# Performance work log

Measured on AMD Instinct MI355X. Metric: run time of the kernel, lower is better.

Reference implementation:

```python
import jax, jax.numpy as jnp
import numpy as np

B, T, DIN, E, H, P = 8, 2048, 256, 256, 4, 8
HD = E // H


def _xavier(key, out_dim, in_dim):
    lim = float(np.sqrt(6.0 / (in_dim + out_dim)))
    return jax.random.uniform(key, (out_dim, in_dim), jnp.float32, -lim, lim)


def setup_inputs() -> dict:
    key = jax.random.key(0)
    ks = jax.random.split(key, 9)
    return {
        "x": jax.random.normal(ks[0], (B, T, DIN), jnp.float32),
        "w_in": _xavier(ks[1], E, DIN), "b_in": jnp.zeros((E,), jnp.float32),
        # MHA in-projections (torch packs qkv; xavier over packed [3E,E] approximated per-slice)
        "w_q": _xavier(ks[2], E, E), "b_q": jnp.zeros((E,), jnp.float32),
        "w_k": _xavier(ks[3], E, E), "b_k": jnp.zeros((E,), jnp.float32),
        "w_v": _xavier(ks[4], E, E), "b_v": jnp.zeros((E,), jnp.float32),
        "w_o": _xavier(ks[5], E, E), "b_o": jnp.zeros((E,), jnp.float32),
        "w_bd": _xavier(ks[6], 1, E), "b_bd": jnp.zeros((1,), jnp.float32),
        "w_pr": _xavier(ks[7], E, E), "b_pr": jnp.zeros((E,), jnp.float32),
    }


def reference(x, w_in, b_in, w_q, b_q, w_k, b_k, w_v, b_v, w_o, b_o, w_bd, b_bd, w_pr, b_pr):
    b, t, _ = x.shape
    h = x @ w_in.T + b_in                                   # [B,T,E]
    # self-attention (batch_first MHA, eval mode -> dropout is identity)
    q = (h @ w_q.T + b_q).reshape(b, t, H, HD)
    k = (h @ w_k.T + b_k).reshape(b, t, H, HD)
    v = (h @ w_v.T + b_v).reshape(b, t, H, HD)
    scale = 1.0 / np.sqrt(HD).astype(np.float32)
    scores = jnp.einsum("bqhd,bkhd->bhqk", q * scale, k)   # [B,H,T,T]
    attn = jax.nn.softmax(scores, axis=-1)
    ao = jnp.einsum("bhqk,bkhd->bqhd", attn, v).reshape(b, t, E)
    ao = ao @ w_o.T + b_o
    # boundary scoring -> dynamic patch ids
    bs = jax.nn.sigmoid(ao @ w_bd.T + b_bd)[..., 0]         # [B,T]
    cum = jnp.cumsum(bs, axis=1)
    normalized = cum / jnp.maximum(cum[:, -1:], 1e-6)
    pid = jnp.minimum((normalized * P).astype(jnp.int32), P - 1)  # [B,T]
    # mean-pool h into P dynamic patches (scatter_add + counts, via one-hot segment matmul)
    oh = jax.nn.one_hot(pid, P, dtype=h.dtype)              # [B,T,P]
    patch_emb = jnp.einsum("btp,btd->bpd", oh, h)           # [B,P,E]
    counts = oh.sum(axis=1)[..., None]                      # [B,P,1]
    patch_emb = patch_emb / jnp.maximum(counts, 1.0)
    return patch_emb @ w_pr.T + b_pr                        # [B,P,E]
```

## Files before the change

### kernel.cpp

```cpp
#include <hip/hip_runtime.h>
#include <cstddef>

#define NB 8
#define NT 2048
#define NE 256
#define NH 4
#define ND 64
#define NP 8

typedef short bf16x8 __attribute__((ext_vector_type(8)));
typedef float f32x4 __attribute__((ext_vector_type(4)));

__device__ __forceinline__ unsigned short f2bf(float f) {
  unsigned u = __builtin_bit_cast(unsigned, f);
  u += 0x7fffu + ((u >> 16) & 1u);
  return (unsigned short)(u >> 16);
}
__device__ __forceinline__ float bf2f(unsigned short h) {
  unsigned u = ((unsigned)h) << 16;
  return __builtin_bit_cast(float, u);
}
__device__ __forceinline__ void split2(float a, float b, unsigned& hi, unsigned& lo) {
  const unsigned short ha = f2bf(a), hb = f2bf(b);
  hi = (unsigned)ha | ((unsigned)hb << 16);
  const unsigned short la = f2bf(a - bf2f(ha));
  const unsigned short lb = f2bf(b - bf2f(hb));
  lo = (unsigned)la | ((unsigned)lb << 16);
}
__device__ __forceinline__ void gld16(const void* g, void* l) {
  __builtin_amdgcn_global_load_lds((const __attribute__((address_space(1))) unsigned*)g,
                                   (__attribute__((address_space(3))) unsigned*)l, 16, 0, 0);
}

#define QSC 0.180336880111120419f

__global__ __launch_bounds__(256) void setup1_kernel(
    const float* __restrict__ w_o, const float* __restrict__ b_o,
    const float* __restrict__ w_bd, const float* __restrict__ b_bd,
    const float* __restrict__ w_v, const float* __restrict__ b_v,
    float* __restrict__ uvbuf, float* __restrict__ consts)
{
  __shared__ float wbd_s[NE];
  __shared__ float u_s[NE];
  const int tid = threadIdx.x;
  wbd_s[tid] = w_bd[tid];
  __syncthreads();
  float a = 0.f;
  for (int j = 0; j < NE; ++j) a = fmaf(wbd_s[j], w_o[j * NE + tid], a);
  u_s[tid] = a;
  __syncthreads();
  #pragma unroll
  for (int hh = 0; hh < NH; ++hh) {
    float a2 = 0.f;
    for (int d = 0; d < ND; ++d)
      a2 = fmaf(u_s[hh * ND + d], w_v[(size_t)(hh * ND + d) * NE + tid], a2);
    uvbuf[hh * NE + tid] = a2;
  }
  if (tid == 0) {
    float cc = 0.f;
    for (int j = 0; j < NE; ++j) cc = fmaf(wbd_s[j], b_o[j], cc);
    consts[0] = cc + b_bd[0];
  }
  if (tid >= 8 && tid < 12) {
    const int hh = tid - 8;
    float cv = 0.f;
    for (int d = 0; d < ND; ++d) cv = fmaf(u_s[hh * ND + d], b_v[hh * ND + d], cv);
    consts[1 + hh] = cv;
  }
}

__global__ __launch_bounds__(256) void setup2_kernel(
    const float* __restrict__ w_in, const float* __restrict__ w_q,
    const float* __restrict__ w_k, const float* __restrict__ b_in,
    const float* __restrict__ b_q, const float* __restrict__ b_k,
    const float* __restrict__ uvbuf, const float* __restrict__ consts,
    unsigned short* __restrict__ wfhi, unsigned short* __restrict__ wflo,
    float* __restrict__ bias_f, float* __restrict__ psum)
{
  const int b = blockIdx.x, tid = threadIdx.x;
  if (b == 97) {
    for (int i = tid; i < NB * NP * NE; i += 256) psum[i] = 0.f;
    return;
  }
  if (b < 32) {
    const int r0 = b * 8;
    #pragma unroll
    for (int j = 0; j < 8; ++j) {
      const int r = r0 + j;
      const float v = w_in[(size_t)r * 256 + tid];
      const unsigned short hb = f2bf(v);
      wfhi[(size_t)r * 256 + tid] = hb;
      wflo[(size_t)r * 256 + tid] = f2bf(v - bf2f(hb));
    }
    if (tid < 8) bias_f[r0 + tid] = b_in[r0 + tid];
    return;
  }
  __shared__ float row8[8][NE];
  __shared__ float b_in_s[NE];
  __shared__ float bias_s[8];
  const int r0 = 256 + (b - 32) * 8;
  b_in_s[tid] = b_in[tid];
  #pragma unroll
  for (int j = 0; j < 8; ++j) {
    const int r = r0 + j;
    float w = 0.f;
    if (r < 512)      w = w_q[(size_t)(r - 256) * 256 + tid];
    else if (r < 768) w = w_k[(size_t)(r - 512) * 256 + tid];
    else if (r < 772) w = uvbuf[(size_t)(r - 768) * 256 + tid];
    row8[j][tid] = w;
  }
  __syncthreads();
  float acc[8] = {};
  for (int e = 0; e < 256; ++e) {
    const float wv = w_in[(size_t)e * 256 + tid];
    #pragma unroll
    for (int j = 0; j < 8; ++j) acc[j] = fmaf(row8[j][e], wv, acc[j]);
  }
  {
    const int g = tid >> 5, l32 = tid & 31;
    float p = 0.f;
    #pragma unroll
    for (int m = 0; m < 8; ++m) p = fmaf(row8[g][l32 + 32 * m], b_in_s[l32 + 32 * m], p);
    p += __shfl_xor(p, 1);  p += __shfl_xor(p, 2);  p += __shfl_xor(p, 4);
    p += __shfl_xor(p, 8);  p += __shfl_xor(p, 16);
    if (l32 == 0) {
      const int r = r0 + g;
      float base = 0.f;
      if (r < 512)      base = b_q[r - 256];
      else if (r < 768) base = b_k[r - 512];
      else if (r < 772) base = consts[1 + (r - 768)];
      float bia = p + base;
      if (r < 512) bia *= QSC;
      bias_s[g] = bia;
    }
  }
  __syncthreads();
  #pragma unroll
  for (int j = 0; j < 8; ++j) {
    const int r = r0 + j;
    if (r >= 772) break;
    float v = acc[j];
    if (r < 512) v *= QSC;
    const unsigned short hb = f2bf(v);
    wfhi[(size_t)r * 256 + tid] = hb;
    wflo[(size_t)r * 256 + tid] = f2bf(v - bf2f(hb));
  }
  if (tid < 8 && r0 + tid < 772) bias_f[r0 + tid] = bias_s[tid];
}

__global__ __launch_bounds__(256) void xgemm_kernel(
    const float* __restrict__ x,
    const unsigned short* __restrict__ wfhi, const unsigned short* __restrict__ wflo,
    const float* __restrict__ bias_f,
    unsigned short* __restrict__ hhi,
    unsigned short* __restrict__ Qhi, unsigned short* __restrict__ Qlo,
    unsigned short* __restrict__ Khi, unsigned short* __restrict__ Klo,
    float* __restrict__ vubuf)
{
  __shared__ __align__(16) char sm[2][24576];
  const int tid = threadIdx.x;
  const int wave = tid >> 6, lane = tid & 63;
  const int lr = lane & 15, lg = lane >> 4;
  const int wm = wave >> 1, wn = wave & 1;
  const int bid = blockIdx.x;
  const int idx = bid >> 3;
  const int m0 = ((bid & 7) * 16 + idx / 13) * 128;
  const int n0 = (idx % 13) * 64;

  const float* aSrc[4];
  #pragma unroll
  for (int c = 0; c < 4; ++c) {
    const int L = c * 4096 + tid * 16;
    const int row = L >> 7, w = (L >> 4) & 7;
    aSrc[c] = x + (size_t)(m0 + row) * 256 + (w ^ (row & 7)) * 4;
  }
  const unsigned short* wSrc[2];
  #pragma unroll
  for (int c = 0; c < 2; ++c) {
    const int L = c * 4096 + tid * 16;
    const int half = (L >> 12) & 1;
    const int Lh = L & 4095;
    const int col = Lh >> 6, w = (Lh >> 4) & 3;
    wSrc[c] = (half ? wflo : wfhi) + (size_t)(n0 + col) * 256 + (w ^ ((col >> 1) & 3)) * 8;
  }
  int aoff[4][2], woff[2];
  #pragma unroll
  for (int s = 0; s < 4; ++s) {
    const int row = wm * 64 + s * 16 + lr;
    const int b0 = row * 128 + lg * 32;
    const int f = (row & 7) << 4;
    aoff[s][0] = b0 ^ f;
    aoff[s][1] = (b0 + 16) ^ f;
  }
  #pragma unroll
  for (int ns = 0; ns < 2; ++ns) {
    const int col = wn * 32 + ns * 16 + lr;
    woff[ns] = (col * 64 + lg * 16) ^ (((col >> 1) & 3) << 4);
  }

  f32x4 acc[4][2];
  #pragma unroll
  for (int s = 0; s < 4; ++s)
    #pragma unroll
    for (int ns = 0; ns < 2; ++ns) acc[s][ns] = (f32x4){0.f, 0.f, 0.f, 0.f};

  {
    char* lb = sm[0];
    #pragma unroll
    for (int c = 0; c < 4; ++c) gld16(aSrc[c], lb + c * 4096 + wave * 1024);
    #pragma unroll
    for (int c = 0; c < 2; ++c) gld16(wSrc[c], lb + 16384 + c * 4096 + wave * 1024);
  }

  for (int kt = 0; kt < 8; ++kt) {
    __syncthreads();
    if (kt < 7) {
      char* nb = sm[(kt + 1) & 1];
      #pragma unroll
      for (int c = 0; c < 4; ++c) gld16(aSrc[c] + (kt + 1) * 32, nb + c * 4096 + wave * 1024);
      #pragma unroll
      for (int c = 0; c < 2; ++c) gld16(wSrc[c] + (kt + 1) * 32, nb + 16384 + c * 4096 + wave * 1024);
    }
    const char* lb = sm[kt & 1];
    bf16x8 ah[4], al[4], wh[2], wl[2];
    #pragma unroll
    for (int s = 0; s < 4; ++s) {
      const f32x4 p0 = *(const f32x4*)(lb + aoff[s][0]);
      const f32x4 p1 = *(const f32x4*)(lb + aoff[s][1]);
      unsigned h0, h1, h2, h3, l0, l1, l2, l3;
      split2(p0[0], p0[1], h0, l0);
      split2(p0[2], p0[3], h1, l1);
      split2(p1[0], p1[1], h2, l2);
      split2(p1[2], p1[3], h3, l3);
      const uint4 hu = make_uint4(h0, h1, h2, h3);
      const uint4 lu = make_uint4(l0, l1, l2, l3);
      ah[s] = __builtin_bit_cast(bf16x8, hu);
      al[s] = __builtin_bit_cast(bf16x8, lu);
    }
    #pragma unroll
    for (int ns = 0; ns < 2; ++ns) {
      wh[ns] = *(const bf16x8*)(lb + 16384 + woff[ns]);
      wl[ns] = *(const bf16x8*)(lb + 20480 + woff[ns]);
    }
    #pragma unroll
    for (int s = 0; s < 4; ++s)
      #pragma unroll
      for (int ns = 0; ns < 2; ++ns) {
        acc[s][ns] = __builtin_amdgcn_mfma_f32_16x16x32_bf16(ah[s], wh[ns], acc[s][ns], 0, 0, 0);
        acc[s][ns] = __builtin_amdgcn_mfma_f32_16x16x32_bf16(ah[s], wl[ns], acc[s][ns], 0, 0, 0);
        acc[s][ns] = __builtin_amdgcn_mfma_f32_16x16x32_bf16(al[s], wh[ns], acc[s][ns], 0, 0, 0);
      }
  }
  #pragma unroll
  for (int s = 0; s < 4; ++s)
    #pragma unroll
    for (int ns = 0; ns < 2; ++ns)
      #pragma unroll
      for (int reg = 0; reg < 4; ++reg) {
        const int row = m0 + wm * 64 + s * 16 + lg * 4 + reg;
        const int col = n0 + wn * 32 + ns * 16 + lr;
        const float v = acc[s][ns][reg] + bias_f[col];
        const int b = row >> 11, t = row & 2047;
        if (col < 256) {
          hhi[(size_t)row * 256 + col] = f2bf(v);
        } else if (col < 768) {
          const int c = (col - 256) & 255;
          const int head = c >> 6, d = c & 63;
          const size_t i2 = (((size_t)(b * NH + head)) * NT + t) * ND + d;
          const unsigned short hb = f2bf(v);
          const unsigned short lb2 = f2bf(v - bf2f(hb));
          if (col < 512) { Qhi[i2] = hb; Qlo[i2] = lb2; }
          else           { Khi[i2] = hb; Klo[i2] = lb2; }
        } else if (col < 772) {
          vubuf[((size_t)(b * NH + (col - 768))) * NT + t] = v;
        }
      }
}

__global__ __launch_bounds__(512) void attn_kernel8(
    const unsigned short* __restrict__ qhi, const unsigned short* __restrict__ qlo,
    const unsigned short* __restrict__ khi, const unsigned short* __restrict__ klo,
    const float* __restrict__ vu, float2* __restrict__ part2)
{
  __shared__ __align__(16) char kbuf[4][16384];
  __shared__ float vu_s[256];
  const int tid = threadIdx.x;
  const int wave = tid >> 6, lane = tid & 63;
  const int lr = lane & 15, lg = lane >> 4;
  const int bid = blockIdx.x;
  const int idx = bid >> 3;
  const int bh = (bid & 7) * 4 + (idx >> 6);
  const int rem = idx & 63;
  const int qt = rem >> 3, kh = rem & 7;
  const size_t base = (size_t)bh * NT * ND;
  const int qrow0 = qt * 256 + wave * 32;
  const int krow0 = kh * 256;

  if (tid < 256) vu_s[tid] = vu[(size_t)bh * NT + krow0 + tid];

  bf16x8 qf[2][2][2];
  #pragma unroll
  for (int s = 0; s < 2; ++s)
    #pragma unroll
    for (int ds = 0; ds < 2; ++ds) {
      const size_t off = base + (size_t)(qrow0 + s * 16 + lr) * ND + ds * 32 + lg * 8;
      qf[s][ds][0] = *(const bf16x8*)(qhi + off);
      qf[s][ds][1] = *(const bf16x8*)(qlo + off);
    }

  const int so = (tid * 16) ^ (((tid >> 3) & 7) << 4);
  int ro0[4], ro1[4];
  #pragma unroll
  for (int ns = 0; ns < 4; ++ns) {
    const int r = ns * 16 + lr;
    const int sw = (r & 7) << 4;
    const int ob = r * 128 + lg * 16;
    ro0[ns] = ob ^ sw;
    ro1[ns] = (ob + 64) ^ sw;
  }
  const char* srcH = (const char*)(khi + base + (size_t)krow0 * ND);
  const char* srcL = (const char*)(klo + base + (size_t)krow0 * ND);
  #pragma unroll
  for (int t = 0; t < 4; ++t) {
    gld16(srcH + t * 8192 + so, &kbuf[t][wave * 1024]);
    gld16(srcL + t * 8192 + so, &kbuf[t][8192 + wave * 1024]);
  }
  __syncthreads();

  float l[8], sv[8];
  #pragma unroll
  for (int i = 0; i < 8; ++i) { l[i] = 0.f; sv[i] = 0.f; }
  const f32x4 Z = (f32x4){0.f, 0.f, 0.f, 0.f};

  #pragma unroll
  for (int it = 0; it < 4; ++it) {
    const int kt = (it + wave) & 3;
    const char* kb = (const char*)kbuf[kt];
    f32x4 acc[2][4];
    float vuv[4];
    __builtin_amdgcn_s_setprio(1);
    #pragma unroll
    for (int ns = 0; ns < 4; ++ns) {
      const bf16x8 kh0 = *(const bf16x8*)(kb + ro0[ns]);
      const bf16x8 kh1 = *(const bf16x8*)(kb + ro1[ns]);
      const bf16x8 kl0 = *(const bf16x8*)(kb + 8192 + ro0[ns]);
      const bf16x8 kl1 = *(const bf16x8*)(kb + 8192 + ro1[ns]);
      vuv[ns] = vu_s[kt * 64 + ns * 16 + lr];
      #pragma unroll
      for (int s = 0; s < 2; ++s) {
        acc[s][ns] = __builtin_amdgcn_mfma_f32_16x16x32_bf16(qf[s][0][0], kh0, Z, 0, 0, 0);
        acc[s][ns] = __builtin_amdgcn_mfma_f32_16x16x32_bf16(qf[s][0][0], kl0, acc[s][ns], 0, 0, 0);
        acc[s][ns] = __builtin_amdgcn_mfma_f32_16x16x32_bf16(qf[s][0][1], kh0, acc[s][ns], 0, 0, 0);
        acc[s][ns] = __builtin_amdgcn_mfma_f32_16x16x32_bf16(qf[s][1][0], kh1, acc[s][ns], 0, 0, 0);
        acc[s][ns] = __builtin_amdgcn_mfma_f32_16x16x32_bf16(qf[s][1][0], kl1, acc[s][ns], 0, 0, 0);
        acc[s][ns] = __builtin_amdgcn_mfma_f32_16x16x32_bf16(qf[s][1][1], kh1, acc[s][ns], 0, 0, 0);
      }
    }
    __builtin_amdgcn_s_setprio(0);
    #pragma unroll
    for (int s = 0; s < 2; ++s)
      #pragma unroll
      for (int reg = 0; reg < 4; ++reg) {
        const int ri = s * 4 + reg;
        #pragma unroll
        for (int ns = 0; ns < 4; ++ns) {
          const float e = __builtin_amdgcn_exp2f(acc[s][ns][reg]);
          l[ri] += e;
          sv[ri] = fmaf(e, vuv[ns], sv[ri]);
        }
      }
  }
  #pragma unroll
  for (int ri = 0; ri < 8; ++ri) {
    #pragma unroll
    for (int off = 1; off < 16; off <<= 1) {
      l[ri]  += __shfl_xor(l[ri],  off, 16);
      sv[ri] += __shfl_xor(sv[ri], off, 16);
    }
  }
  if (lr == 0) {
    #pragma unroll
    for (int s = 0; s < 2; ++s)
      #pragma unroll
      for (int reg = 0; reg < 4; ++reg) {
        const int row = qrow0 + s * 16 + lg * 4 + reg;
        part2[(((size_t)bh * NT + row) << 3) + kh] = make_float2(l[s * 4 + reg], sv[s * 4 + reg]);
      }
  }
}

__global__ __launch_bounds__(256) void combine_kernel(
    const float4* __restrict__ part4, const float* __restrict__ consts,
    float* __restrict__ bs)
{
  const int gid = blockIdx.x * 256 + threadIdx.x;
  const int b = gid >> 11, t = gid & 2047;
  float logit = consts[0];
  #pragma unroll
  for (int hh = 0; hh < NH; ++hh) {
    const size_t p0 = ((size_t)((b * NH + hh) * NT) + t) * 4;
    float lsum = 0.f, ssum = 0.f;
    #pragma unroll
    for (int q = 0; q < 4; ++q) {
      const float4 p = part4[p0 + q];
      lsum += p.x + p.z;
      ssum += p.y + p.w;
    }
    logit += ssum / lsum;
  }
  bs[gid] = 1.f / (1.f + expf(-logit));
}

__global__ __launch_bounds__(256) void boundary_kernel(
    const float* __restrict__ bs, int* __restrict__ pid, int* __restrict__ counts)
{
  const int b = blockIdx.x, tid = threadIdx.x;
  __shared__ float partial[256];
  __shared__ int cnt_s[8];
  float v[8];
  float run = 0.f;
  const float4 b0 = *(const float4*)(bs + b * NT + tid * 8);
  const float4 b1 = *(const float4*)(bs + b * NT + tid * 8 + 4);
  const float bv[8] = {b0.x, b0.y, b0.z, b0.w, b1.x, b1.y, b1.z, b1.w};
  #pragma unroll
  for (int i = 0; i < 8; ++i) { run += bv[i]; v[i] = run; }
  float x = run;
  partial[tid] = x;
  __syncthreads();
  for (int off = 1; off < 256; off <<= 1) {
    const float y = (tid >= off) ? partial[tid - off] : 0.f;
    __syncthreads();
    x += y;
    partial[tid] = x;
    __syncthreads();
  }
  const float total = partial[255];
  if (tid < 8) cnt_s[tid] = 0;
  __syncthreads();
  const float denom = fmaxf(total, 1e-6f);
  const float excl = x - run;
  #pragma unroll
  for (int i = 0; i < 8; ++i) {
    const float norm = (excl + v[i]) / denom;
    int pp = (int)(norm * 8.f);
    pp = pp > 7 ? 7 : pp;
    pid[b * NT + tid * 8 + i] = pp;
    atomicAdd(&cnt_s[pp], 1);
  }
  __syncthreads();
  if (tid < 8) counts[b * 8 + tid] = cnt_s[tid];
}

__global__ __launch_bounds__(256) void pool_kernel(
    const unsigned short* __restrict__ hhi, const int* __restrict__ pid,
    float* __restrict__ psum)
{
  const int b = blockIdx.x >> 4, chunk = blockIdx.x & 15;
  const int tid = threadIdx.x;
  __shared__ int pid_s[128];
  const int t0 = chunk * 128;
  if (tid < 128) pid_s[tid] = pid[b * NT + t0 + tid];
  __syncthreads();
  float acc[8] = {};
  for (int tok = 0; tok < 128; ++tok) {
    const float val = bf2f(hhi[((size_t)b * NT + t0 + tok) * NE + tid]);
    const int p = pid_s[tok];
    #pragma unroll
    for (int pp = 0; pp < 8; ++pp) acc[pp] += (p == pp) ? val : 0.f;
  }
  #pragma unroll
  for (int pp = 0; pp < 8; ++pp)
    atomicAdd(&psum[((size_t)b * NP + pp) * NE + tid], acc[pp]);
}

__global__ __launch_bounds__(256) void final_kernel(
    const float* __restrict__ psum, const int* __restrict__ counts,
    const float* __restrict__ w_pr, const float* __restrict__ b_pr, float* __restrict__ out)
{
  const int bp = blockIdx.x;
  const int tid = threadIdx.x;
  __shared__ float pe[NE];
  const float cnt = fmaxf((float)counts[bp], 1.f);
  pe[tid] = psum[(size_t)bp * NE + tid] / cnt;
  __syncthreads();
  float acc = 0.f;
  for (int e = 0; e < NE; ++e) acc = fmaf(pe[e], w_pr[(size_t)tid * NE + e], acc);
  out[(size_t)bp * NE + tid] = acc + b_pr[tid];
}

extern "C" void kernel_launch(void* const* d_in, const int* in_sizes, int n_in,
                              void* d_out, int out_size, void* d_ws, size_t ws_size,
                              hipStream_t stream) {
  (void)in_sizes; (void)n_in; (void)out_size; (void)ws_size;
  const float* x    = (const float*)d_in[0];
  const float* w_in = (const float*)d_in[1];
  const float* b_in = (const float*)d_in[2];
  const float* w_q  = (const float*)d_in[3];
  const float* b_q  = (const float*)d_in[4];
  const float* w_k  = (const float*)d_in[5];
  const float* b_k  = (const float*)d_in[6];
  const float* w_v  = (const float*)d_in[7];
  const float* b_v  = (const float*)d_in[8];
  const float* w_o  = (const float*)d_in[9];
  const float* b_o  = (const float*)d_in[10];
  const float* w_bd = (const float*)d_in[11];
  const float* b_bd = (const float*)d_in[12];
  const float* w_pr = (const float*)d_in[13];
  const float* b_pr = (const float*)d_in[14];
  float* out = (float*)d_out;

  const size_t M = (size_t)NB * NT;
  unsigned short* hhi = (unsigned short*)d_ws;
  unsigned short* qhi = hhi + M * NE;
  unsigned short* qlo = qhi + M * NE;
  unsigned short* khi = qlo + M * NE;
  unsigned short* klo = khi + M * NE;
  unsigned short* wfhi = klo + M * NE;
  unsigned short* wflo = wfhi + 212992;
  float* bias_f = (float*)(wflo + 212992);
  float* uvbuf  = bias_f + 832;
  float* vubuf  = uvbuf + 1024;
  float* part   = vubuf + 65536;
  float* bsbuf  = part + 1048576;
  float* consts = bsbuf + 16384;
  float* psum   = consts + 8;
  int*   pid    = (int*)(psum + 16384);
  int*   counts = pid + 16384;

  setup1_kernel<<<1, 256, 0, stream>>>(w_o, b_o, w_bd, b_bd, w_v, b_v, uvbuf, consts);
  setup2_kernel<<<98, 256, 0, stream>>>(w_in, w_q, w_k, b_in, b_q, b_k,
      uvbuf, consts, wfhi, wflo, bias_f, psum);
  xgemm_kernel<<<1664, 256, 0, stream>>>(x, wfhi, wflo, bias_f,
      hhi, qhi, qlo, khi, klo, vubuf);
  attn_kernel8<<<2048, 512, 0, stream>>>(qhi, qlo, khi, klo, vubuf, (float2*)part);
  combine_kernel<<<64, 256, 0, stream>>>((const float4*)part, consts, bsbuf);
  boundary_kernel<<<8, 256, 0, stream>>>(bsbuf, pid, counts);
  pool_kernel<<<128, 256, 0, stream>>>(hhi, pid, psum);
  final_kernel<<<64, 256, 0, stream>>>(psum, counts, w_pr, b_pr, out);
}
```

Baseline: 171.1 us.

## Split fp32 x into bf16 hi/lo once at staging instead of per-wave reads

In the fused input/QKV projection GEMM, the A tile (x, fp32) is no longer copied straight into LDS and split into bf16 hi/lo by every reading wave. Each thread now loads its slice of x into registers and splits it once. It writes the hi/lo bf16 halves into LDS after the MFMAs of the current k-step, so the global load overlaps with compute. This removes redundant split work across waves and halves the A-tile LDS read traffic, at the cost of extra registers and a register-staged rather than async global-to-LDS path.

```diff
diff --git a/kernel.cpp b/kernel.cpp
--- a/kernel.cpp
+++ b/kernel.cpp
@@ -167,13 +167,13 @@
   const int m0 = ((bid & 7) * 16 + idx / 13) * 128;
   const int n0 = (idx % 13) * 64;
 
-  const float* aSrc[4];
-  #pragma unroll
-  for (int c = 0; c < 4; ++c) {
-    const int L = c * 4096 + tid * 16;
-    const int row = L >> 7, w = (L >> 4) & 7;
-    aSrc[c] = x + (size_t)(m0 + row) * 256 + (w ^ (row & 7)) * 4;
-  }
+  const int arow = tid >> 1;
+  const int acolh = (tid & 1) * 16;
+  const float* axp = x + (size_t)(m0 + arow) * 256 + acolh;
+  const int asw = ((arow >> 1) & 3) << 4;
+  const int aw0 = (arow * 64 + acolh * 2) ^ asw;
+  const int aw1 = (arow * 64 + acolh * 2 + 16) ^ asw;
+
   const unsigned short* wSrc[2];
   #pragma unroll
   for (int c = 0; c < 2; ++c) {
@@ -183,14 +183,11 @@
     const int col = Lh >> 6, w = (Lh >> 4) & 3;
     wSrc[c] = (half ? wflo : wfhi) + (size_t)(n0 + col) * 256 + (w ^ ((col >> 1) & 3)) * 8;
   }
-  int aoff[4][2], woff[2];
+  int aoff[4], woff[2];
   #pragma unroll
   for (int s = 0; s < 4; ++s) {
     const int row = wm * 64 + s * 16 + lr;
-    const int b0 = row * 128 + lg * 32;
-    const int f = (row & 7) << 4;
-    aoff[s][0] = b0 ^ f;
-    aoff[s][1] = (b0 + 16) ^ f;
+    aoff[s] = (row * 64 + lg * 16) ^ (((row >> 1) & 3) << 4);
   }
   #pragma unroll
   for (int ns = 0; ns < 2; ++ns) {
@@ -204,38 +201,40 @@
     #pragma unroll
     for (int ns = 0; ns < 2; ++ns) acc[s][ns] = (f32x4){0.f, 0.f, 0.f, 0.f};
 
+  f32x4 ar[4];
+  #pragma unroll
+  for (int j = 0; j < 4; ++j) ar[j] = *(const f32x4*)(axp + j * 4);
   {
     char* lb = sm[0];
     #pragma unroll
-    for (int c = 0; c < 4; ++c) gld16(aSrc[c], lb + c * 4096 + wave * 1024);
-    #pragma unroll
     for (int c = 0; c < 2; ++c) gld16(wSrc[c], lb + 16384 + c * 4096 + wave * 1024);
-  }
+    unsigned h[8], l[8];
+    #pragma unroll
+    for (int j = 0; j < 4; ++j) {
+      split2(ar[j][0], ar[j][1], h[j * 2], l[j * 2]);
+      split2(ar[j][2], ar[j][3], h[j * 2 + 1], l[j * 2 + 1]);
+    }
+    *(uint4*)(lb + aw0)        = make_uint4(h[0], h[1], h[2], h[3]);
+    *(uint4*)(lb + aw1)        = make_uint4(h[4], h[5], h[6], h[7]);
+    *(uint4*)(lb + 8192 + aw0) = make_uint4(l[0], l[1], l[2], l[3]);
+    *(uint4*)(lb + 8192 + aw1) = make_uint4(l[4], l[5], l[6], l[7]);
+  }
+  __syncthreads();
 
   for (int kt = 0; kt < 8; ++kt) {
-    __syncthreads();
+    const char* lb = sm[kt & 1];
+    char* nb = sm[(kt + 1) & 1];
     if (kt < 7) {
-      char* nb = sm[(kt + 1) & 1];
-      #pragma unroll
-      for (int c = 0; c < 4; ++c) gld16(aSrc[c] + (kt + 1) * 32, nb + c * 4096 + wave * 1024);
       #pragma unroll
       for (int c = 0; c < 2; ++c) gld16(wSrc[c] + (kt + 1) * 32, nb + 16384 + c * 4096 + wave * 1024);
-    }
-    const char* lb = sm[kt & 1];
+      #pragma unroll
+      for (int j = 0; j < 4; ++j) ar[j] = *(const f32x4*)(axp + (kt + 1) * 32 + j * 4);
+    }
     bf16x8 ah[4], al[4], wh[2], wl[2];
     #pragma unroll
     for (int s = 0; s < 4; ++s) {
-      const f32x4 p0 = *(const f32x4*)(lb + aoff[s][0]);
-      const f32x4 p1 = *(const f32x4*)(lb + aoff[s][1]);
-      unsigned h0, h1, h2, h3, l0, l1, l2, l3;
-      split2(p0[0], p0[1], h0, l0);
-      split2(p0[2], p0[3], h1, l1);
-      split2(p1[0], p1[1], h2, l2);
-      split2(p1[2], p1[3], h3, l3);
-      const uint4 hu = make_uint4(h0, h1, h2, h3);
-      const uint4 lu = make_uint4(l0, l1, l2, l3);
-      ah[s] = __builtin_bit_cast(bf16x8, hu);
-      al[s] = __builtin_bit_cast(bf16x8, lu);
+      ah[s] = *(const bf16x8*)(lb + aoff[s]);
+      al[s] = *(const bf16x8*)(lb + 8192 + aoff[s]);
     }
     #pragma unroll
     for (int ns = 0; ns < 2; ++ns) {
@@ -250,6 +249,19 @@
         acc[s][ns] = __builtin_amdgcn_mfma_f32_16x16x32_bf16(ah[s], wl[ns], acc[s][ns], 0, 0, 0);
         acc[s][ns] = __builtin_amdgcn_mfma_f32_16x16x32_bf16(al[s], wh[ns], acc[s][ns], 0, 0, 0);
       }
+    if (kt < 7) {
+      unsigned h[8], l[8];
+      #pragma unroll
+      for (int j = 0; j < 4; ++j) {
+        split2(ar[j][0], ar[j][1], h[j * 2], l[j * 2]);
+        split2(ar[j][2], ar[j][3], h[j * 2 + 1], l[j * 2 + 1]);
+      }
+      *(uint4*)(nb + aw0)        = make_uint4(h[0], h[1], h[2], h[3]);
+      *(uint4*)(nb + aw1)        = make_uint4(h[4], h[5], h[6], h[7]);
+      *(uint4*)(nb + 8192 + aw0) = make_uint4(l[0], l[1], l[2], l[3]);
+      *(uint4*)(nb + 8192 + aw1) = make_uint4(l[4], l[5], l[6], l[7]);
+    }
+    __syncthreads();
   }
   #pragma unroll
   for (int s = 0; s < 4; ++s)
```

Result: faster. 166.8 us (-2.5%).

## Pre-split x into bf16 hi/lo and widen xgemm N tile to 128

Applied to the files above, without the earlier changes.

Adds a separate kernel that converts x into bf16 hi/lo planes once, so the GEMM no longer re-splits fp32 A tiles in its inner loop for every N tile. The xgemm N tile doubles from 64 to 128 columns, with the weight matrix padded to 896 rows and zeroed, which halves the number of blocks and the times A is reloaded. This costs an extra launch plus write and read of the x split buffers, more accumulator registers, and 64KB of LDS per block, which may lower occupancy.

```diff
diff --git a/kernel.cpp b/kernel.cpp
--- a/kernel.cpp
+++ b/kernel.cpp
@@ -19,13 +19,6 @@
 __device__ __forceinline__ float bf2f(unsigned short h) {
   unsigned u = ((unsigned)h) << 16;
   return __builtin_bit_cast(float, u);
-}
-__device__ __forceinline__ void split2(float a, float b, unsigned& hi, unsigned& lo) {
-  const unsigned short ha = f2bf(a), hb = f2bf(b);
-  hi = (unsigned)ha | ((unsigned)hb << 16);
-  const unsigned short la = f2bf(a - bf2f(ha));
-  const unsigned short lb = f2bf(b - bf2f(hb));
-  lo = (unsigned)la | ((unsigned)lb << 16);
 }
 __device__ __forceinline__ void gld16(const void* g, void* l) {
   __builtin_amdgcn_global_load_lds((const __attribute__((address_space(1))) unsigned*)g,
@@ -80,6 +73,14 @@
   const int b = blockIdx.x, tid = threadIdx.x;
   if (b == 97) {
     for (int i = tid; i < NB * NP * NE; i += 256) psum[i] = 0.f;
+    return;
+  }
+  if (b == 98) {
+    for (int r = 772; r < 896; ++r) {
+      wfhi[(size_t)r * 256 + tid] = 0;
+      wflo[(size_t)r * 256 + tid] = 0;
+    }
+    if (tid < 124) bias_f[772 + tid] = 0.f;
     return;
   }
   if (b < 32) {
@@ -148,8 +149,31 @@
   if (tid < 8 && r0 + tid < 772) bias_f[r0 + tid] = bias_s[tid];
 }
 
+__global__ __launch_bounds__(256) void xsplit_kernel(
+    const float* __restrict__ x, unsigned short* __restrict__ xhi,
+    unsigned short* __restrict__ xlo)
+{
+  const int i0 = blockIdx.x * 512 + threadIdx.x;
+  #pragma unroll
+  for (int rep = 0; rep < 2; ++rep) {
+    const int i = i0 + rep * 256;
+    const float4 v = *(const float4*)(x + (size_t)i * 4);
+    const float vv[4] = {v.x, v.y, v.z, v.w};
+    unsigned short h4[4], l4[4];
+    #pragma unroll
+    for (int j = 0; j < 4; ++j) {
+      h4[j] = f2bf(vv[j]);
+      l4[j] = f2bf(vv[j] - bf2f(h4[j]));
+    }
+    *(ushort2*)(xhi + (size_t)i * 4)     = make_ushort2(h4[0], h4[1]);
+    *(ushort2*)(xhi + (size_t)i * 4 + 2) = make_ushort2(h4[2], h4[3]);
+    *(ushort2*)(xlo + (size_t)i * 4)     = make_ushort2(l4[0], l4[1]);
+    *(ushort2*)(xlo + (size_t)i * 4 + 2) = make_ushort2(l4[2], l4[3]);
+  }
+}
+
 __global__ __launch_bounds__(256) void xgemm_kernel(
-    const float* __restrict__ x,
+    const unsigned short* __restrict__ xhi, const unsigned short* __restrict__ xlo,
     const unsigned short* __restrict__ wfhi, const unsigned short* __restrict__ wflo,
     const float* __restrict__ bias_f,
     unsigned short* __restrict__ hhi,
@@ -157,59 +181,53 @@
     unsigned short* __restrict__ Khi, unsigned short* __restrict__ Klo,
     float* __restrict__ vubuf)
 {
-  __shared__ __align__(16) char sm[2][24576];
+  __shared__ __align__(16) char sm[2][32768];
   const int tid = threadIdx.x;
   const int wave = tid >> 6, lane = tid & 63;
   const int lr = lane & 15, lg = lane >> 4;
   const int wm = wave >> 1, wn = wave & 1;
   const int bid = blockIdx.x;
   const int idx = bid >> 3;
-  const int m0 = ((bid & 7) * 16 + idx / 13) * 128;
-  const int n0 = (idx % 13) * 64;
-
-  const float* aSrc[4];
+  const int m0 = ((bid & 7) * 16 + idx / 7) * 128;
+  const int n0 = (idx % 7) * 128;
+
+  const unsigned short* aSrc[4];
+  const unsigned short* wSrc[4];
   #pragma unroll
   for (int c = 0; c < 4; ++c) {
     const int L = c * 4096 + tid * 16;
-    const int row = L >> 7, w = (L >> 4) & 7;
-    aSrc[c] = x + (size_t)(m0 + row) * 256 + (w ^ (row & 7)) * 4;
-  }
-  const unsigned short* wSrc[2];
-  #pragma unroll
-  for (int c = 0; c < 2; ++c) {
-    const int L = c * 4096 + tid * 16;
-    const int half = (L >> 12) & 1;
-    const int Lh = L & 4095;
-    const int col = Lh >> 6, w = (Lh >> 4) & 3;
-    wSrc[c] = (half ? wflo : wfhi) + (size_t)(n0 + col) * 256 + (w ^ ((col >> 1) & 3)) * 8;
-  }
-  int aoff[4][2], woff[2];
+    const int half = L >> 13;
+    const int Lh = L & 8191;
+    const int row = Lh >> 6, w = (Lh >> 4) & 3;
+    const int g = (w ^ ((row >> 1) & 3)) * 8;
+    aSrc[c] = (half ? xlo : xhi) + (size_t)(m0 + row) * 256 + g;
+    wSrc[c] = (half ? wflo : wfhi) + (size_t)(n0 + row) * 256 + g;
+  }
+  int aoff[4], woff[4];
   #pragma unroll
   for (int s = 0; s < 4; ++s) {
     const int row = wm * 64 + s * 16 + lr;
-    const int b0 = row * 128 + lg * 32;
-    const int f = (row & 7) << 4;
-    aoff[s][0] = b0 ^ f;
-    aoff[s][1] = (b0 + 16) ^ f;
-  }
-  #pragma unroll
-  for (int ns = 0; ns < 2; ++ns) {
-    const int col = wn * 32 + ns * 16 + lr;
+    aoff[s] = (row * 64 + lg * 16) ^ (((row >> 1) & 3) << 4);
+  }
+  #pragma unroll
+  for (int ns = 0; ns < 4; ++ns) {
+    const int col = wn * 64 + ns * 16 + lr;
     woff[ns] = (col * 64 + lg * 16) ^ (((col >> 1) & 3) << 4);
   }
 
-  f32x4 acc[4][2];
+  f32x4 acc[4][4];
   #pragma unroll
   for (int s = 0; s < 4; ++s)
     #pragma unroll
-    for (int ns = 0; ns < 2; ++ns) acc[s][ns] = (f32x4){0.f, 0.f, 0.f, 0.f};
+    for (int ns = 0; ns < 4; ++ns) acc[s][ns] = (f32x4){0.f, 0.f, 0.f, 0.f};
 
   {
     char* lb = sm[0];
     #pragma unroll
-    for (int c = 0; c < 4; ++c) gld16(aSrc[c], lb + c * 4096 + wave * 1024);
-    #pragma unroll
-    for (int c = 0; c < 2; ++c) gld16(wSrc[c], lb + 16384 + c * 4096 + wave * 1024);
+    for (int c = 0; c < 4; ++c) {
+      gld16(aSrc[c], lb + c * 4096 + wave * 1024);
+      gld16(wSrc[c], lb + 16384 + c * 4096 + wave * 1024);
+    }
   }
 
   for (int kt = 0; kt < 8; ++kt) {
@@ -217,35 +235,27 @@
     if (kt < 7) {
       char* nb = sm[(kt + 1) & 1];
       #pragma unroll
-      for (int c = 0; c < 4; ++c) gld16(aSrc[c] + (kt + 1) * 32, nb + c * 4096 + wave * 1024);
-      #pragma unroll
-      for (int c = 0; c < 2; ++c) gld16(wSrc[c] + (kt + 1) * 32, nb + 16384 + c * 4096 + wave * 1024);
+      for (int c = 0; c < 4; ++c) {
+        gld16(aSrc[c] + (kt + 1) * 32, nb + c * 4096 + wave * 1024);
+        gld16(wSrc[c] + (kt + 1) * 32, nb + 16384 + c * 4096 + wave * 1024);
+      }
     }
     const char* lb = sm[kt & 1];
-    bf16x8 ah[4], al[4], wh[2], wl[2];
+    bf16x8 ah[4], al[4], wh[4], wl[4];
     #pragma unroll
     for (int s = 0; s < 4; ++s) {
-      const f32x4 p0 = *(const f32x4*)(lb + aoff[s][0]);
-      const f32x4 p1 = *(const f32x4*)(lb + aoff[s][1]);
-      unsigned h0, h1, h2, h3, l0, l1, l2, l3;
-      split2(p0[0], p0[1], h0, l0);
-      split2(p0[2], p0[3], h1, l1);
-      split2(p1[0], p1[1], h2, l2);
-      split2(p1[2], p1[3], h3, l3);
-      const uint4 hu = make_uint4(h0, h1, h2, h3);
-      const uint4 lu = make_uint4(l0, l1, l2, l3);
-      ah[s] = __builtin_bit_cast(bf16x8, hu);
-      al[s] = __builtin_bit_cast(bf16x8, lu);
-    }
-    #pragma unroll
-    for (int ns = 0; ns < 2; ++ns) {
+      ah[s] = *(const bf16x8*)(lb + aoff[s]);
+      al[s] = *(const bf16x8*)(lb + 8192 + aoff[s]);
+    }
+    #pragma unroll
+    for (int ns = 0; ns < 4; ++ns) {
       wh[ns] = *(const bf16x8*)(lb + 16384 + woff[ns]);
-      wl[ns] = *(const bf16x8*)(lb + 20480 + woff[ns]);
+      wl[ns] = *(const bf16x8*)(lb + 24576 + woff[ns]);
     }
     #pragma unroll
     for (int s = 0; s < 4; ++s)
       #pragma unroll
-      for (int ns = 0; ns < 2; ++ns) {
+      for (int ns = 0; ns < 4; ++ns) {
         acc[s][ns] = __builtin_amdgcn_mfma_f32_16x16x32_bf16(ah[s], wh[ns], acc[s][ns], 0, 0, 0);
         acc[s][ns] = __builtin_amdgcn_mfma_f32_16x16x32_bf16(ah[s], wl[ns], acc[s][ns], 0, 0, 0);
         acc[s][ns] = __builtin_amdgcn_mfma_f32_16x16x32_bf16(al[s], wh[ns], acc[s][ns], 0, 0, 0);
@@ -254,11 +264,12 @@
   #pragma unroll
   for (int s = 0; s < 4; ++s)
     #pragma unroll
-    for (int ns = 0; ns < 2; ++ns)
+    for (int ns = 0; ns < 4; ++ns)
       #pragma unroll
       for (int reg = 0; reg < 4; ++reg) {
         const int row = m0 + wm * 64 + s * 16 + lg * 4 + reg;
-        const int col = n0 + wn * 32 + ns * 16 + lr;
+        const int col = n0 + wn * 64 + ns * 16 + lr;
+        if (col >= 772) continue;
         const float v = acc[s][ns][reg] + bias_f[col];
         const int b = row >> 11, t = row & 2047;
         if (col < 256) {
@@ -271,7 +282,7 @@
           const unsigned short lb2 = f2bf(v - bf2f(hb));
           if (col < 512) { Qhi[i2] = hb; Qlo[i2] = lb2; }
           else           { Khi[i2] = hb; Klo[i2] = lb2; }
-        } else if (col < 772) {
+        } else {
           vubuf[((size_t)(b * NH + (col - 768))) * NT + t] = v;
         }
       }
@@ -515,10 +526,12 @@
   unsigned short* qlo = qhi + M * NE;
   unsigned short* khi = qlo + M * NE;
   unsigned short* klo = khi + M * NE;
-  unsigned short* wfhi = klo + M * NE;
-  unsigned short* wflo = wfhi + 212992;
-  float* bias_f = (float*)(wflo + 212992);
-  float* uvbuf  = bias_f + 832;
+  unsigned short* xhi = klo + M * NE;
+  unsigned short* xlo = xhi + M * NE;
+  unsigned short* wfhi = xlo + M * NE;
+  unsigned short* wflo = wfhi + 229376;
+  float* bias_f = (float*)(wflo + 229376);
+  float* uvbuf  = bias_f + 896;
   float* vubuf  = uvbuf + 1024;
   float* part   = vubuf + 65536;
   float* bsbuf  = part + 1048576;
@@ -528,9 +541,10 @@
   int*   counts = pid + 16384;
 
   setup1_kernel<<<1, 256, 0, stream>>>(w_o, b_o, w_bd, b_bd, w_v, b_v, uvbuf, consts);
-  setup2_kernel<<<98, 256, 0, stream>>>(w_in, w_q, w_k, b_in, b_q, b_k,
+  setup2_kernel<<<99, 256, 0, stream>>>(w_in, w_q, w_k, b_in, b_q, b_k,
       uvbuf, consts, wfhi, wflo, bias_f, psum);
-  xgemm_kernel<<<1664, 256, 0, stream>>>(x, wfhi, wflo, bias_f,
+  xsplit_kernel<<<2048, 256, 0, stream>>>(x, xhi, xlo);
+  xgemm_kernel<<<896, 256, 0, stream>>>(xhi, xlo, wfhi, wflo, bias_f,
       hhi, qhi, qlo, khi, klo, vubuf);
   attn_kernel8<<<2048, 512, 0, stream>>>(qhi, qlo, khi, klo, vubuf, (float2*)part);
   combine_kernel<<<64, 256, 0, stream>>>((const float4*)part, consts, bsbuf);
```

After: 169.9 us. Within noise of the previous version (-0.7%).
